# Performance work log

Hardware: AMD Instinct MI355X
Metric: run time of the kernel (lower is better)

## Reference

```python
import jax, jax.numpy as jnp
import numpy as np

N_SOURCES = 2      # n_sources == n_clusters
N_ITERS = 100      # iter_clustering default in apply_kmeans


def setup_inputs() -> dict:
    key = jax.random.key(0)
    # (batch, n_sources, latent_dim, T) -- speaker_stack output, feature_last=False
    spk_vector = jax.random.normal(key, (4, 2, 512, 16000), dtype=jnp.float32)
    return {"spk_vector": spk_vector}


def _kmeans(x):
    # x: (B, T, S, D); 100 iterations of WaveSplit's per-frame k-means.
    def step(x, _):
        # torch: centroids = x.mean(dim=1, keepdim=True) -> mean over time T
        cent = x.mean(axis=1)                                   # (B, S, D)
        # pairwise distances ||x[b,t,s] - cent[b,c]||; argmin over c is
        # invariant to sqrt, so use the squared-distance expansion (no BTSSD tensor)
        x2 = jnp.sum(x * x, axis=-1)                            # (B, T, S)
        c2 = jnp.sum(cent * cent, axis=-1)                      # (B, S)
        dot = jnp.einsum('btsd,bcd->btsc', x, cent)             # (B, T, S, S)
        dist2 = x2[..., None] + c2[:, None, None, :] - 2.0 * dot
        idx = jnp.argmin(dist2, axis=3)                         # (B, T, S)
        mask = jax.nn.one_hot(idx, N_SOURCES, dtype=x.dtype)    # (B, T, S, C)
        # torch: sum(mask.unsqueeze(4) * x.unsqueeze(3), dim=2) -> sum members into clusters
        x_new = jnp.einsum('btsc,btsd->btcd', mask, x)          # (B, T, C, D)
        return x_new, None

    x, _ = jax.lax.scan(step, x, None, length=N_ITERS)
    return x


def reference(spk_vector):
    # apply_kmeans(spk_vector, feature_last=False)
    x = jnp.transpose(spk_vector, (0, 3, 1, 2))   # (B, T, S, D)
    x = _kmeans(x)
    return jnp.transpose(x, (0, 2, 3, 1))         # (B, S, D, T)
```

## Files before the change

### kernel.cpp

```cpp
#include <hip/hip_runtime.h>

#define NB 4
#define ND 512
#define NT 16000
#define NITERS 100
#define DS 8
#define DCH 64
#define TCH 16
#define FPC 1000
#define FPT 4
#define APT 250

__device__ __align__(16) unsigned char g_states[NB * NT];
__device__ float4 g_nfin[NB * NT];
__device__ float4 g_npart[NB * DS * NT];
__device__ float4 g_pdot[NB * DS * NT];
__device__ float g_Spart[NB * DS * TCH * 2 * DCH];
__device__ int g_changed[NITERS + 1];

__device__ __forceinline__ float4 ld4(const float* p) { return *(const float4*)p; }

#define WREDUCE2(a0, a1)                     \
  _Pragma("unroll")                          \
  for (int m = 1; m < 64; m <<= 1) {         \
    a0 += __shfl_xor(a0, m);                 \
    a1 += __shfl_xor(a1, m);                 \
  }

#define MKW(st_, w0_, w1_)                   \
  do { w0_ = (st_ == 0) || (st_ == 2);       \
       w1_ = (st_ == 1) || (st_ == 2); } while (0)

__global__ __launch_bounds__(256) void init_kernel(const float* __restrict__ in) {
  int j = blockIdx.x, tc = blockIdx.y, b = blockIdx.z, tid = threadIdx.x;
  int wave = tid >> 6, lane = tid & 63;
  bool act = tid < APT;
  int t0 = tc * FPC + tid * FPT;
  int t0c = act ? t0 : 0;
  float msk = act ? 1.f : 0.f;
  __shared__ float accw[4][2][DCH];
  const float* base0 = in + ((size_t)(b * 2 + 0) * ND) * NT;
  const float* base1 = in + ((size_t)(b * 2 + 1) * ND) * NT;
  float4 q00 = {0, 0, 0, 0}, q11 = {0, 0, 0, 0}, qs = {0, 0, 0, 0};
#pragma unroll 2
  for (int dl = 0; dl < DCH; ++dl) {
    int d = j * DCH + dl;
    float4 v0 = ld4(base0 + (size_t)d * NT + t0c);
    float4 v1 = ld4(base1 + (size_t)d * NT + t0c);
    v0.x *= msk; v0.y *= msk; v0.z *= msk; v0.w *= msk;
    v1.x *= msk; v1.y *= msk; v1.z *= msk; v1.w *= msk;
    q00.x = fmaf(v0.x, v0.x, q00.x); q00.y = fmaf(v0.y, v0.y, q00.y);
    q00.z = fmaf(v0.z, v0.z, q00.z); q00.w = fmaf(v0.w, v0.w, q00.w);
    q11.x = fmaf(v1.x, v1.x, q11.x); q11.y = fmaf(v1.y, v1.y, q11.y);
    q11.z = fmaf(v1.z, v1.z, q11.z); q11.w = fmaf(v1.w, v1.w, q11.w);
    float sx = v0.x + v1.x, sy = v0.y + v1.y, sz = v0.z + v1.z, sw = v0.w + v1.w;
    qs.x = fmaf(sx, sx, qs.x); qs.y = fmaf(sy, sy, qs.y);
    qs.z = fmaf(sz, sz, qs.z); qs.w = fmaf(sw, sw, qs.w);
    float a0 = (v0.x + v0.y) + (v0.z + v0.w);
    float a1 = (v1.x + v1.y) + (v1.z + v1.w);
    WREDUCE2(a0, a1)
    if (lane == 0) { accw[wave][0][dl] = a0; accw[wave][1][dl] = a1; }
  }
  __syncthreads();
  if (tid < 2 * DCH) {
    int c = tid >> 6, dl = tid & 63;
    g_Spart[(((size_t)(b * DS + j) * TCH + tc) * 2 + c) * DCH + dl] =
        ((accw[0][c][dl] + accw[1][c][dl]) + accw[2][c][dl]) + accw[3][c][dl];
  }
  if (act) {
    size_t pb = (size_t)(b * DS + j) * NT + t0;
    g_npart[pb + 0] = make_float4(q00.x, q11.x, qs.x, 0.f);
    g_npart[pb + 1] = make_float4(q00.y, q11.y, qs.y, 0.f);
    g_npart[pb + 2] = make_float4(q00.z, q11.z, qs.z, 0.f);
    g_npart[pb + 3] = make_float4(q00.w, q11.w, qs.w, 0.f);
  }
  if (j == 0 && act) *(uchar4*)&g_states[(size_t)b * NT + t0] = make_uchar4(0, 0, 0, 0);
  if (j == 0 && tc == 0 && b == 0)
    for (int i = tid; i <= NITERS; i += 256) g_changed[i] = (i == 0) ? 1 : 0;
}

__global__ __launch_bounds__(256) void init2_kernel() {
  int blk = blockIdx.x, b = blockIdx.y;
  int t = blk * 256 + (int)threadIdx.x;
  if (t >= NT) return;
  float n00 = 0.f, n11 = 0.f, ns = 0.f;
  for (int jj = 0; jj < DS; ++jj) {
    float4 p = g_npart[(size_t)(b * DS + jj) * NT + t];
    n00 += p.x; n11 += p.y; ns += p.z;
  }
  g_nfin[(size_t)b * NT + t] = make_float4(n00, n11, ns, 0.f);
}

__global__ __launch_bounds__(256) void dots_kernel(const float* __restrict__ in, int iter) {
  if (g_changed[iter] == 0) return;
  int j = blockIdx.x, tc = blockIdx.y, b = blockIdx.z, tid = threadIdx.x;
  __shared__ float cl[2][DCH];
  if (tid < 2 * DCH) {
    int c = tid >> 6, dl = tid & 63;
    float s = 0.f;
    for (int p = 0; p < TCH; ++p)
      s += g_Spart[(((size_t)(b * DS + j) * TCH + p) * 2 + c) * DCH + dl];
    cl[c][dl] = s / (float)NT;
  }
  __syncthreads();
  bool act = tid < APT;
  int t0 = tc * FPC + tid * FPT;
  int t0c = act ? t0 : 0;
  const float* base0 = in + ((size_t)(b * 2 + 0) * ND) * NT;
  const float* base1 = in + ((size_t)(b * 2 + 1) * ND) * NT;
  float4 g00 = {0,0,0,0}, g01 = {0,0,0,0}, g10 = {0,0,0,0}, g11 = {0,0,0,0};
#pragma unroll 4
  for (int dl = 0; dl < DCH; ++dl) {
    int d = j * DCH + dl;
    float4 v0 = ld4(base0 + (size_t)d * NT + t0c);
    float4 v1 = ld4(base1 + (size_t)d * NT + t0c);
    float c0 = cl[0][dl], c1 = cl[1][dl];
    g00.x = fmaf(v0.x, c0, g00.x); g00.y = fmaf(v0.y, c0, g00.y);
    g00.z = fmaf(v0.z, c0, g00.z); g00.w = fmaf(v0.w, c0, g00.w);
    g01.x = fmaf(v0.x, c1, g01.x); g01.y = fmaf(v0.y, c1, g01.y);
    g01.z = fmaf(v0.z, c1, g01.z); g01.w = fmaf(v0.w, c1, g01.w);
    g10.x = fmaf(v1.x, c0, g10.x); g10.y = fmaf(v1.y, c0, g10.y);
    g10.z = fmaf(v1.z, c0, g10.z); g10.w = fmaf(v1.w, c0, g10.w);
    g11.x = fmaf(v1.x, c1, g11.x); g11.y = fmaf(v1.y, c1, g11.y);
    g11.z = fmaf(v1.z, c1, g11.z); g11.w = fmaf(v1.w, c1, g11.w);
  }
  if (act) {
    size_t pb = (size_t)(b * DS + j) * NT + t0;
    g_pdot[pb + 0] = make_float4(g00.x, g01.x, g10.x, g11.x);
    g_pdot[pb + 1] = make_float4(g00.y, g01.y, g10.y, g11.y);
    g_pdot[pb + 2] = make_float4(g00.z, g01.z, g10.z, g11.z);
    g_pdot[pb + 3] = make_float4(g00.w, g01.w, g10.w, g11.w);
  }
}

__global__ __launch_bounds__(256) void upd_kernel(int iter) {
  if (g_changed[iter] == 0) return;
  int blk = blockIdx.x, b = blockIdx.y, tid = threadIdx.x;
  __shared__ float clf[2 * ND];
  __shared__ float c2s[2];
  for (int i = tid; i < 2 * ND; i += 256) {
    int c = i >> 9, d = i & 511;
    int jj = d >> 6, dl = d & 63;
    float s = 0.f;
    for (int p = 0; p < TCH; ++p)
      s += g_Spart[(((size_t)(b * DS + jj) * TCH + p) * 2 + c) * DCH + dl];
    clf[i] = s / (float)NT;
  }
  __syncthreads();
  int lane = tid & 63;
  if (tid < 64) {
    float q0 = 0.f, q1 = 0.f;
    for (int d = lane; d < ND; d += 64) {
      float a = clf[d], e = clf[ND + d];
      q0 += a * a; q1 += e * e;
    }
    WREDUCE2(q0, q1)
    if (lane == 0) { c2s[0] = q0; c2s[1] = q1; }
  }
  __syncthreads();
  int t = blk * 256 + tid;
  if (t >= NT) return;
  size_t f = (size_t)b * NT + t;
  float g00 = 0.f, g01 = 0.f, g10 = 0.f, g11 = 0.f;
  for (int jj = 0; jj < DS; ++jj) {
    float4 p = g_pdot[(size_t)(b * DS + jj) * NT + t];
    g00 += p.x; g01 += p.y; g10 += p.z; g11 += p.w;
  }
  float4 nf = g_nfin[f];
  float a00 = nf.x, a11 = nf.y, asum = nf.z;
  unsigned char st_old = (unsigned char)(g_states[f] & 3);
  float x2_0, x2_1, d00, d01, d10, d11;
  switch (st_old) {
    case 0: x2_0 = a00;  x2_1 = a11;  d00 = g00;       d01 = g01;       d10 = g10;       d11 = g11;       break;
    case 1: x2_0 = a11;  x2_1 = a00;  d00 = g10;       d01 = g11;       d10 = g00;       d11 = g01;       break;
    case 2: x2_0 = asum; x2_1 = 0.f;  d00 = g00 + g10; d01 = g01 + g11; d10 = 0.f;       d11 = 0.f;       break;
    default: x2_0 = 0.f; x2_1 = asum; d00 = 0.f;       d01 = 0.f;       d10 = g00 + g10; d11 = g01 + g11; break;
  }
  float c2_0 = c2s[0], c2_1 = c2s[1];
  float dist00 = (x2_0 + c2_0) - 2.f * d00;
  float dist01 = (x2_0 + c2_1) - 2.f * d01;
  float dist10 = (x2_1 + c2_0) - 2.f * d10;
  float dist11 = (x2_1 + c2_1) - 2.f * d11;
  int i0 = (dist00 <= dist01) ? 0 : 1;
  int i1 = (dist10 <= dist11) ? 0 : 1;
  unsigned char st_new;
  if (i0 == 0 && i1 == 0) st_new = 2;
  else if (i0 == 1 && i1 == 1) st_new = 3;
  else if (i0 == 0) st_new = st_old;
  else st_new = (unsigned char)(st_old ^ 1);
  g_states[f] = st_new;
  if (st_new != st_old) g_changed[iter + 1] = 1;
}

__global__ __launch_bounds__(256) void csum_kernel(const float* __restrict__ in, int iter) {
  if (g_changed[iter + 1] == 0) return;
  int j = blockIdx.x, tc = blockIdx.y, b = blockIdx.z, tid = threadIdx.x;
  int wave = tid >> 6, lane = tid & 63;
  bool act = tid < APT;
  int t0 = tc * FPC + tid * FPT;
  int t0c = act ? t0 : 0;
  float msk = act ? 1.f : 0.f;
  __shared__ float accw[4][2][DCH];
  uchar4 st = *(const uchar4*)&g_states[(size_t)b * NT + t0c];
  bool w00, w10, w01, w11, w02, w12, w03, w13;
  MKW(st.x, w00, w10); MKW(st.y, w01, w11); MKW(st.z, w02, w12); MKW(st.w, w03, w13);
  const float* base0 = in + ((size_t)(b * 2 + 0) * ND) * NT;
  const float* base1 = in + ((size_t)(b * 2 + 1) * ND) * NT;
#pragma unroll 2
  for (int dl = 0; dl < DCH; ++dl) {
    int d = j * DCH + dl;
    float4 v0 = ld4(base0 + (size_t)d * NT + t0c);
    float4 v1 = ld4(base1 + (size_t)d * NT + t0c);
    v0.x *= msk; v0.y *= msk; v0.z *= msk; v0.w *= msk;
    v1.x *= msk; v1.y *= msk; v1.z *= msk; v1.w *= msk;
    float p0x = (w00 ? v0.x : 0.f) + (w10 ? v1.x : 0.f);
    float p1x = (w00 ? 0.f : v0.x) + (w10 ? 0.f : v1.x);
    float p0y = (w01 ? v0.y : 0.f) + (w11 ? v1.y : 0.f);
    float p1y = (w01 ? 0.f : v0.y) + (w11 ? 0.f : v1.y);
    float p0z = (w02 ? v0.z : 0.f) + (w12 ? v1.z : 0.f);
    float p1z = (w02 ? 0.f : v0.z) + (w12 ? 0.f : v1.z);
    float p0w = (w03 ? v0.w : 0.f) + (w13 ? v1.w : 0.f);
    float p1w = (w03 ? 0.f : v0.w) + (w13 ? 0.f : v1.w);
    float a0 = (p0x + p0y) + (p0z + p0w);
    float a1 = (p1x + p1y) + (p1z + p1w);
    WREDUCE2(a0, a1)
    if (lane == 0) { accw[wave][0][dl] = a0; accw[wave][1][dl] = a1; }
  }
  __syncthreads();
  if (tid < 2 * DCH) {
    int c = tid >> 6, dl = tid & 63;
    g_Spart[(((size_t)(b * DS + j) * TCH + tc) * 2 + c) * DCH + dl] =
        ((accw[0][c][dl] + accw[1][c][dl]) + accw[2][c][dl]) + accw[3][c][dl];
  }
}

__global__ __launch_bounds__(256) void output_kernel(const float* __restrict__ in,
                                                     float* __restrict__ out) {
  int j = blockIdx.x, tc = blockIdx.y, b = blockIdx.z, tid = threadIdx.x;
  if (tid >= APT) return;
  int t0 = tc * FPC + tid * FPT;
  uchar4 st = *(const uchar4*)&g_states[(size_t)b * NT + t0];
  bool w00, w10, w01, w11, w02, w12, w03, w13;
  MKW(st.x, w00, w10); MKW(st.y, w01, w11); MKW(st.z, w02, w12); MKW(st.w, w03, w13);
  const float* b0 = in + ((size_t)(b * 2 + 0) * ND) * NT;
  const float* b1 = in + ((size_t)(b * 2 + 1) * ND) * NT;
  float* o0 = out + ((size_t)(b * 2 + 0) * ND) * NT;
  float* o1 = out + ((size_t)(b * 2 + 1) * ND) * NT;
#pragma unroll 2
  for (int dl = 0; dl < DCH; ++dl) {
    int d = j * DCH + dl;
    float4 v0 = ld4(b0 + (size_t)d * NT + t0);
    float4 v1 = ld4(b1 + (size_t)d * NT + t0);
    float4 a0, a1;
    a0.x = (w00 ? v0.x : 0.f) + (w10 ? v1.x : 0.f);
    a1.x = (w00 ? 0.f : v0.x) + (w10 ? 0.f : v1.x);
    a0.y = (w01 ? v0.y : 0.f) + (w11 ? v1.y : 0.f);
    a1.y = (w01 ? 0.f : v0.y) + (w11 ? 0.f : v1.y);
    a0.z = (w02 ? v0.z : 0.f) + (w12 ? v1.z : 0.f);
    a1.z = (w02 ? 0.f : v0.z) + (w12 ? 0.f : v1.z);
    a0.w = (w03 ? v0.w : 0.f) + (w13 ? v1.w : 0.f);
    a1.w = (w03 ? 0.f : v0.w) + (w13 ? 0.f : v1.w);
    *(float4*)(o0 + (size_t)d * NT + t0) = a0;
    *(float4*)(o1 + (size_t)d * NT + t0) = a1;
  }
}

extern "C" void kernel_launch(void* const* d_in, const int* in_sizes, int n_in,
                              void* d_out, int out_size, void* d_ws, size_t ws_size,
                              hipStream_t stream) {
  const float* in = (const float*)d_in[0];
  float* out = (float*)d_out;
  (void)d_ws; (void)ws_size; (void)in_sizes; (void)n_in; (void)out_size;

  dim3 g3(DS, TCH, NB), b256(256);
  init_kernel<<<g3, b256, 0, stream>>>(in);
  init2_kernel<<<dim3(63, NB), b256, 0, stream>>>();
  for (int i = 0; i < NITERS; ++i) {
    dots_kernel<<<g3, b256, 0, stream>>>(in, i);
    upd_kernel<<<dim3(63, NB), b256, 0, stream>>>(i);
    if (i < NITERS - 1) csum_kernel<<<g3, b256, 0, stream>>>(in, i);
  }
  output_kernel<<<g3, b256, 0, stream>>>(in, out);
}
```

Measured before the change: 5.320 ms.

## Skip csum work per wave when its frame chunk has no state changes

```diff
diff --git a/kernel.cpp b/kernel.cpp
--- a/kernel.cpp
+++ b/kernel.cpp
@@ -10,15 +10,21 @@
 #define FPC 1000
 #define FPT 4
 #define APT 250
+#define NWCH 64
 
 __device__ __align__(16) unsigned char g_states[NB * NT];
 __device__ float4 g_nfin[NB * NT];
 __device__ float4 g_npart[NB * DS * NT];
 __device__ float4 g_pdot[NB * DS * NT];
-__device__ float g_Spart[NB * DS * TCH * 2 * DCH];
+__device__ float g_Spart[(size_t)NB * DS * NWCH * 2 * DCH];
+__device__ unsigned char g_chflag[(size_t)(NITERS + 1) * NB * NWCH];
 __device__ int g_changed[NITERS + 1];
 
 __device__ __forceinline__ float4 ld4(const float* p) { return *(const float4*)p; }
+
+__device__ __forceinline__ size_t SP(int b, int j, int p, int c, int dl) {
+  return (((size_t)(b * DS + j) * NWCH + p) * 2 + c) * DCH + dl;
+}
 
 #define WREDUCE2(a0, a1)                     \
   _Pragma("unroll")                          \
@@ -38,10 +44,10 @@
   int t0 = tc * FPC + tid * FPT;
   int t0c = act ? t0 : 0;
   float msk = act ? 1.f : 0.f;
-  __shared__ float accw[4][2][DCH];
   const float* base0 = in + ((size_t)(b * 2 + 0) * ND) * NT;
   const float* base1 = in + ((size_t)(b * 2 + 1) * ND) * NT;
   float4 q00 = {0, 0, 0, 0}, q11 = {0, 0, 0, 0}, qs = {0, 0, 0, 0};
+  float r0 = 0.f, r1 = 0.f;
 #pragma unroll 2
   for (int dl = 0; dl < DCH; ++dl) {
     int d = j * DCH + dl;
@@ -59,14 +65,11 @@
     float a0 = (v0.x + v0.y) + (v0.z + v0.w);
     float a1 = (v1.x + v1.y) + (v1.z + v1.w);
     WREDUCE2(a0, a1)
-    if (lane == 0) { accw[wave][0][dl] = a0; accw[wave][1][dl] = a1; }
-  }
-  __syncthreads();
-  if (tid < 2 * DCH) {
-    int c = tid >> 6, dl = tid & 63;
-    g_Spart[(((size_t)(b * DS + j) * TCH + tc) * 2 + c) * DCH + dl] =
-        ((accw[0][c][dl] + accw[1][c][dl]) + accw[2][c][dl]) + accw[3][c][dl];
-  }
+    if (lane == dl) { r0 = a0; r1 = a1; }
+  }
+  int p = tc * 4 + wave;
+  g_Spart[SP(b, j, p, 0, lane)] = r0;
+  g_Spart[SP(b, j, p, 1, lane)] = r1;
   if (act) {
     size_t pb = (size_t)(b * DS + j) * NT + t0;
     g_npart[pb + 0] = make_float4(q00.x, q11.x, qs.x, 0.f);
@@ -75,8 +78,11 @@
     g_npart[pb + 3] = make_float4(q00.w, q11.w, qs.w, 0.f);
   }
   if (j == 0 && act) *(uchar4*)&g_states[(size_t)b * NT + t0] = make_uchar4(0, 0, 0, 0);
-  if (j == 0 && tc == 0 && b == 0)
+  if (j == 0 && tc == 0 && b == 0) {
     for (int i = tid; i <= NITERS; i += 256) g_changed[i] = (i == 0) ? 1 : 0;
+    for (size_t i = tid; i < (size_t)(NITERS + 1) * NB * NWCH; i += 256)
+      g_chflag[i] = 0;
+  }
 }
 
 __global__ __launch_bounds__(256) void init2_kernel() {
@@ -98,8 +104,7 @@
   if (tid < 2 * DCH) {
     int c = tid >> 6, dl = tid & 63;
     float s = 0.f;
-    for (int p = 0; p < TCH; ++p)
-      s += g_Spart[(((size_t)(b * DS + j) * TCH + p) * 2 + c) * DCH + dl];
+    for (int p = 0; p < NWCH; ++p) s += g_Spart[SP(b, j, p, c, dl)];
     cl[c][dl] = s / (float)NT;
   }
   __syncthreads();
@@ -142,8 +147,7 @@
     int c = i >> 9, d = i & 511;
     int jj = d >> 6, dl = d & 63;
     float s = 0.f;
-    for (int p = 0; p < TCH; ++p)
-      s += g_Spart[(((size_t)(b * DS + jj) * TCH + p) * 2 + c) * DCH + dl];
+    for (int p = 0; p < NWCH; ++p) s += g_Spart[SP(b, jj, p, c, dl)];
     clf[i] = s / (float)NT;
   }
   __syncthreads();
@@ -189,23 +193,31 @@
   else if (i0 == 0) st_new = st_old;
   else st_new = (unsigned char)(st_old ^ 1);
   g_states[f] = st_new;
-  if (st_new != st_old) g_changed[iter + 1] = 1;
+  if (st_new != st_old) {
+    g_changed[iter + 1] = 1;
+    int tcc = t / FPC;
+    int w = (t - tcc * FPC) >> 8;
+    g_chflag[(size_t)(iter + 1) * NB * NWCH + b * NWCH + tcc * 4 + w] = 1;
+  }
 }
 
 __global__ __launch_bounds__(256) void csum_kernel(const float* __restrict__ in, int iter) {
   if (g_changed[iter + 1] == 0) return;
   int j = blockIdx.x, tc = blockIdx.y, b = blockIdx.z, tid = threadIdx.x;
   int wave = tid >> 6, lane = tid & 63;
+  int p = tc * 4 + wave;
+  if (g_chflag[(size_t)(iter + 1) * NB * NWCH + b * NWCH + p] == 0)
+    return;
   bool act = tid < APT;
   int t0 = tc * FPC + tid * FPT;
   int t0c = act ? t0 : 0;
   float msk = act ? 1.f : 0.f;
-  __shared__ float accw[4][2][DCH];
   uchar4 st = *(const uchar4*)&g_states[(size_t)b * NT + t0c];
   bool w00, w10, w01, w11, w02, w12, w03, w13;
   MKW(st.x, w00, w10); MKW(st.y, w01, w11); MKW(st.z, w02, w12); MKW(st.w, w03, w13);
   const float* base0 = in + ((size_t)(b * 2 + 0) * ND) * NT;
   const float* base1 = in + ((size_t)(b * 2 + 1) * ND) * NT;
+  float r0 = 0.f, r1 = 0.f;
 #pragma unroll 2
   for (int dl = 0; dl < DCH; ++dl) {
     int d = j * DCH + dl;
@@ -224,14 +236,10 @@
     float a0 = (p0x + p0y) + (p0z + p0w);
     float a1 = (p1x + p1y) + (p1z + p1w);
     WREDUCE2(a0, a1)
-    if (lane == 0) { accw[wave][0][dl] = a0; accw[wave][1][dl] = a1; }
-  }
-  __syncthreads();
-  if (tid < 2 * DCH) {
-    int c = tid >> 6, dl = tid & 63;
-    g_Spart[(((size_t)(b * DS + j) * TCH + tc) * 2 + c) * DCH + dl] =
-        ((accw[0][c][dl] + accw[1][c][dl]) + accw[2][c][dl]) + accw[3][c][dl];
-  }
+    if (lane == dl) { r0 = a0; r1 = a1; }
+  }
+  g_Spart[SP(b, j, p, 0, lane)] = r0;
+  g_Spart[SP(b, j, p, 1, lane)] = r1;
 }
 
 __global__ __launch_bounds__(256) void output_kernel(const float* __restrict__ in,
```

New measurement: 4.562 ms. 14.2% less time.
